# Optimization experiments

Hardware: AMD Instinct MI355X
Metric: run time of the kernel (lower is better)

The kernel has to match this reference:

```python
import jax, jax.numpy as jnp
import numpy as np

B, T, D = 2, 2048, 1024
H = 16
HD = D // H  # head dim == config.k == config.v == 64


def setup_inputs() -> dict:
    key = jax.random.key(0)
    k1, k2, k3 = jax.random.split(key, 3)
    scale = 0.02
    x = jax.random.normal(k1, (B, T, D), dtype=jnp.float32)
    W1 = jax.random.normal(k2, (D, 3 * D), dtype=jnp.float32) * scale
    b1 = jnp.zeros((3 * D,), dtype=jnp.float32)
    W2 = jax.random.normal(k3, (D, D), dtype=jnp.float32) * scale
    b2 = jnp.zeros((D,), dtype=jnp.float32)
    return {"x": x, "W1": W1, "b1": b1, "W2": W2, "b2": b2}


def reference(x, W1, b1, W2, b2):
    # Fused QKV projection (dropout layers are identity in eval mode).
    Bx, Tx, C = x.shape
    qkv = x @ W1 + b1                      # [B, T, 3D]
    q, k, v = jnp.split(qkv, 3, axis=-1)   # each [B, T, D]
    q = q.reshape(Bx, Tx, H, HD).transpose(0, 2, 1, 3)  # [B, H, T, hd]
    k = k.reshape(Bx, Tx, H, HD).transpose(0, 2, 1, 3)
    v = v.reshape(Bx, Tx, H, HD).transpose(0, 2, 1, 3)

    logits = jnp.einsum('bhmk,bhnk->bhmn', q, k) / jnp.sqrt(jnp.float32(HD))
    # causal mask (lower-triangular bias buffer)
    causal = jnp.tril(jnp.ones((Tx, Tx), dtype=bool))
    logits = jnp.where(causal[None, None], logits, jnp.float32(-jnp.inf))
    att = jax.nn.softmax(logits, axis=-1)   # [B, H, T, T]

    y = jnp.einsum('bhmn,bhnv->bhmv', att, v)        # [B, H, T, hd]
    y = y.transpose(0, 2, 1, 3).reshape(Bx, Tx, C)   # [B, T, D]
    return y @ W2 + b2
```

## Files before the change

kernel.cpp:

```cpp
#include <hip/hip_runtime.h>

typedef __attribute__((ext_vector_type(8))) short bf16x8;
typedef __attribute__((ext_vector_type(4))) float f32x4;
typedef __attribute__((ext_vector_type(16))) float f32x16;
typedef __attribute__((ext_vector_type(4))) short short4v;
typedef __attribute__((ext_vector_type(4))) unsigned int uint4v;

#define B_  2
#define T_  2048
#define D_  1024
#define H_  16
#define HD_ 64

__device__ inline short f2bf(float f){
  unsigned u = __builtin_bit_cast(unsigned, f);
  u += 0x7fff + ((u >> 16) & 1);
  return (short)(u >> 16);
}
__device__ inline float bf2f(short s){
  unsigned u = ((unsigned)(unsigned short)s) << 16;
  return __builtin_bit_cast(float, u);
}

__device__ inline void gl2lds16(const void* g, void* l){
  __builtin_amdgcn_global_load_lds(
      (const __attribute__((address_space(1))) unsigned int*)g,
      (__attribute__((address_space(3))) unsigned int*)l, 16, 0, 0);
}

__device__ inline void transpose_tile(const float* __restrict__ in,
                                      short* __restrict__ out,
                                      int R, int C, int bx, int by){
  __shared__ float tile[32][33];
  int tx = threadIdx.x & 31, ty0 = threadIdx.x >> 5;
#pragma unroll
  for (int i = 0; i < 4; i++){
    int ty = ty0 + i * 8;
    tile[ty][tx] = in[(by + ty) * C + bx + tx];
  }
  __syncthreads();
#pragma unroll
  for (int i = 0; i < 4; i++){
    int ty = ty0 + i * 8;
    out[(bx + ty) * R + by + tx] = f2bf(tile[tx][ty]);
  }
}

__global__ __launch_bounds__(256) void prep(
    const float* __restrict__ x,  short* __restrict__ xb,
    const float* __restrict__ W1, short* __restrict__ W1T,
    const float* __restrict__ W2, short* __restrict__ W2T){
  const int bid = blockIdx.x;
  if (bid < 4096){
    int i = (bid * 256 + threadIdx.x) * 4;
    float4 v = *(const float4*)(x + i);
    short4v o;
    o[0] = f2bf(v.x); o[1] = f2bf(v.y); o[2] = f2bf(v.z); o[3] = f2bf(v.w);
    *(short4v*)(xb + i) = o;
  } else if (bid < 4096 + 3072){
    int tb = bid - 4096;
    transpose_tile(W1, W1T, 1024, 3072, (tb % 96) << 5, (tb / 96) << 5);
  } else {
    int tb = bid - 7168;
    transpose_tile(W2, W2T, 1024, 1024, (tb % 32) << 5, (tb / 32) << 5);
  }
}

#define QSCALE 0.18033688011112042f

__global__ __launch_bounds__(512) void gemm_qkv8(
    const short* __restrict__ A, const short* __restrict__ Bt,
    const float* __restrict__ bias,
    short* __restrict__ q, short* __restrict__ kk, short* __restrict__ vT){
  constexpr int K_ = 1024, NT = K_ / 64;
  __shared__ short As[2][256 * 64];
  __shared__ short Bs[2][256 * 64];
  const int tid = threadIdx.x;
  const int lane = tid & 63, w = tid >> 6;
  const int wm = w >> 2, wn = w & 3;
  const int lr = lane & 15, lk = lane >> 4;
  const int brow = blockIdx.y * 256, bcol = blockIdx.x * 256;
  const short* Ag = A  + brow * K_;
  const short* Bg = Bt + bcol * K_;
  f32x4 acc[8][4] = {};

  auto stageA = [&](int buf, int k0){
#pragma unroll
    for (int j = 0; j < 4; j++){
      int row = wm * 128 + wn * 32 + j * 8 + (lane >> 3);
      int colb = (lane & 7) * 16;
      int cs = colb ^ ((row & 7) << 4);
      gl2lds16(Ag + row * K_ + k0 + (cs >> 1), (char*)As[buf] + row * 128 + colb);
    }
  };
  auto stageB = [&](int buf, int k0){
#pragma unroll
    for (int j = 0; j < 4; j++){
      int row = (wn >> 1) * 128 + (wm * 2 + (wn & 1)) * 32 + j * 8 + (lane >> 3);
      int colb = (lane & 7) * 16;
      int cs = colb ^ ((row & 7) << 4);
      gl2lds16(Bg + row * K_ + k0 + (cs >> 1), (char*)Bs[buf] + row * 128 + colb);
    }
  };

  bf16x8 aF[8], bF[4], bF2[4];
  auto loadA = [&](const short* Ac, int r){
#pragma unroll
    for (int mf = 0; mf < 4; mf++){
      int row = wm * 128 + r * 64 + mf * 16 + lr;
      const char* rp = (const char*)Ac + row * 128;
      int swz = (row & 7) << 4;
#pragma unroll
      for (int kx = 0; kx < 2; kx++)
        aF[mf * 2 + kx] = *(const bf16x8*)(rp + ((kx * 64 + lk * 16) ^ swz));
    }
  };
  auto loadB = [&](const short* Bc, int c, bf16x8* dst){
#pragma unroll
    for (int nf = 0; nf < 2; nf++){
      int row = wn * 64 + c * 32 + nf * 16 + lr;
      const char* rp = (const char*)Bc + row * 128;
      int swz = (row & 7) << 4;
#pragma unroll
      for (int kx = 0; kx < 2; kx++)
        dst[nf * 2 + kx] = *(const bf16x8*)(rp + ((kx * 64 + lk * 16) ^ swz));
    }
  };

#define MFMA_SUB(r, c, B)                                                    \
  __builtin_amdgcn_s_setprio(1);                                             \
  _Pragma("unroll")                                                          \
  for (int mf = 0; mf < 4; mf++)                                             \
    _Pragma("unroll")                                                        \
    for (int nf = 0; nf < 2; nf++)                                           \
      _Pragma("unroll")                                                      \
      for (int kx = 0; kx < 2; kx++)                                         \
        acc[(r)*4 + mf][(c)*2 + nf] = __builtin_amdgcn_mfma_f32_16x16x32_bf16(\
            aF[mf*2+kx], (B)[nf*2+kx], acc[(r)*4 + mf][(c)*2 + nf], 0, 0, 0);\
  __builtin_amdgcn_s_setprio(0);

  stageA(0, 0);
  stageB(0, 0);

  for (int t = 0; t < NT; ++t){
    const int cur = t & 1, nxt = cur ^ 1;
    const short* Ac = As[cur];
    const short* Bc = Bs[cur];
    const bool pf = (t + 1 < NT);
    asm volatile("s_waitcnt vmcnt(0)" ::: "memory");
    __builtin_amdgcn_s_barrier();
    __builtin_amdgcn_sched_barrier(0);
    loadA(Ac, 0);
    loadB(Bc, 0, bF);
    if (pf) stageA(nxt, (t + 1) * 64);
    __builtin_amdgcn_sched_barrier(0);
    __builtin_amdgcn_s_barrier();
    __builtin_amdgcn_sched_barrier(0);
    MFMA_SUB(0, 0, bF)
    __builtin_amdgcn_sched_barrier(0);
    __builtin_amdgcn_s_barrier();
    loadB(Bc, 1, bF2);
    if (pf) stageB(nxt, (t + 1) * 64);
    __builtin_amdgcn_sched_barrier(0);
    __builtin_amdgcn_s_barrier();
    __builtin_amdgcn_sched_barrier(0);
    MFMA_SUB(0, 1, bF2)
    __builtin_amdgcn_sched_barrier(0);
    __builtin_amdgcn_s_barrier();
    loadA(Ac, 1);
    __builtin_amdgcn_sched_barrier(0);
    __builtin_amdgcn_s_barrier();
    __builtin_amdgcn_sched_barrier(0);
    MFMA_SUB(1, 0, bF)
    __builtin_amdgcn_sched_barrier(0);
    __builtin_amdgcn_s_barrier();
    MFMA_SUB(1, 1, bF2)
    __builtin_amdgcn_sched_barrier(0);
  }

#pragma unroll
  for (int nf = 0; nf < 4; nf++){
    int n = bcol + wn * 64 + nf * 16 + lr;
    float bv = bias[n];
    int sec = n >> 10, d = n & 1023, h = d >> 6, hd = d & 63;
#pragma unroll
    for (int qd = 0; qd < 8; qd++){
      int m0 = brow + wm * 128 + qd * 16 + lk * 4;
      int bb = m0 >> 11, t0 = m0 & 2047;
      int bh = bb * H_ + h;
      if (sec == 0){
#pragma unroll
        for (int r = 0; r < 4; r++)
          q[(bh * T_ + t0 + r) * HD_ + hd] = f2bf((acc[qd][nf][r] + bv) * QSCALE);
      } else if (sec == 1){
#pragma unroll
        for (int r = 0; r < 4; r++)
          kk[(bh * T_ + t0 + r) * HD_ + hd] = f2bf(acc[qd][nf][r] + bv);
      } else {
        float v0 = acc[qd][nf][0] + bv, v1 = acc[qd][nf][1] + bv;
        float v2 = acc[qd][nf][2] + bv, v3 = acc[qd][nf][3] + bv;
        unsigned lo = (unsigned)(unsigned short)f2bf(v0) | ((unsigned)(unsigned short)f2bf(v1) << 16);
        unsigned hi = (unsigned)(unsigned short)f2bf(v2) | ((unsigned)(unsigned short)f2bf(v3) << 16);
        uint2 pk; pk.x = lo; pk.y = hi;
        *(uint2*)(vT + (bh * HD_ + hd) * T_ + t0) = pk;
      }
    }
  }
}

#define BM 128
#define BN 128
#define BK 32

template<int N_, int K_>
__global__ __launch_bounds__(256, 3) void gemm_bt(
    const short* __restrict__ A, const short* __restrict__ Bt,
    const float* __restrict__ bias, float* __restrict__ outf){
  __shared__ short As[3][BM * BK];
  __shared__ short Bs[3][BN * BK];
  const int tid = threadIdx.x;
  const int lane = tid & 63, w = tid >> 6;
  const int wm = w >> 1, wn = w & 1;
  const int lr = lane & 15, lk = lane >> 4;
  const int brow = blockIdx.y * BM, bcol = blockIdx.x * BN;
  f32x4 acc[4][4] = {};
  const short* Ag = A  + brow * K_;
  const short* Bg = Bt + bcol * K_;

  auto stage = [&](int buf, int k0){
#pragma unroll
    for (int i = 0; i < 2; i++){
      int idx = i * 256 + tid;
      int row = idx >> 2, c8 = (idx & 3) * 8;
      gl2lds16(Ag + row * K_ + k0 + c8, (char*)As[buf] + idx * 16);
      gl2lds16(Bg + row * K_ + k0 + c8, (char*)Bs[buf] + idx * 16);
    }
  };

  const int NT = K_ / BK;
  stage(0, 0);
  stage(1, BK);
  for (int t = 0; t < NT; ++t){
    if (t + 1 < NT)
      asm volatile("s_waitcnt vmcnt(4)" ::: "memory");
    else
      asm volatile("s_waitcnt vmcnt(0)" ::: "memory");
    __builtin_amdgcn_s_barrier();
    __builtin_amdgcn_sched_barrier(0);
    if (t + 2 < NT)
      stage((t + 2) % 3, (t + 2) * BK);
    __builtin_amdgcn_sched_barrier(0);

    const short* Ac = As[t % 3];
    const short* Bc = Bs[t % 3];
    bf16x8 a[4], b[4];
#pragma unroll
    for (int mf = 0; mf < 4; mf++)
      a[mf] = *(const bf16x8*)(Ac + (wm * 64 + mf * 16 + lr) * BK + lk * 8);
#pragma unroll
    for (int nf = 0; nf < 4; nf++)
      b[nf] = *(const bf16x8*)(Bc + (wn * 64 + nf * 16 + lr) * BK + lk * 8);
    __builtin_amdgcn_s_setprio(1);
#pragma unroll
    for (int mf = 0; mf < 4; mf++)
#pragma unroll
      for (int nf = 0; nf < 4; nf++)
        acc[mf][nf] = __builtin_amdgcn_mfma_f32_16x16x32_bf16(a[mf], b[nf], acc[mf][nf], 0, 0, 0);
    __builtin_amdgcn_s_setprio(0);
  }

#pragma unroll
  for (int nf = 0; nf < 4; nf++){
    int n = bcol + wn * 64 + nf * 16 + lr;
    float bv = bias[n];
#pragma unroll
    for (int mf = 0; mf < 4; mf++){
      int m0 = brow + wm * 64 + mf * 16 + lk * 4;
#pragma unroll
      for (int r = 0; r < 4; r++)
        outf[(m0 + r) * N_ + n] = acc[mf][nf][r] + bv;
    }
  }
}

__device__ inline int crow(int r, int h){ return (r & 3) + 8 * (r >> 2) + 4 * h; }

template<int NS>
__global__ __launch_bounds__(256, 4) void attn32(
    const short* __restrict__ Q, const short* __restrict__ Kg,
    const short* __restrict__ Vt, short* __restrict__ Y,
    short* __restrict__ Op, float* __restrict__ ml){
  __shared__ short Ks[2][64 * 64];
  __shared__ short Vs[2][64 * 64];
  __shared__ float bounce[4][32];
  const int tid = threadIdx.x;
  const int w = tid >> 6, l = tid & 63;
  const int lq = l & 31, h = l >> 5;
  const int bx = blockIdx.x;
  int i, hf;
  if constexpr (NS == 4){
    int u = bx >> 5, v = u & 15;
    i = (v < 8) ? 15 - v : v - 8;
    hf = u >> 4;
  } else {
    i = (bx < 256) ? 15 - (bx >> 5) : (bx >> 5) - 8;
    hf = 0;
  }
  const int bh = bx & 31;
  const int q0 = i * 128, qw = q0 + w * 32;
  const int nt = 2 * (i + 1);
  const int t0 = hf * nt / NS;
  const int t1 = (hf + 1) * nt / NS;

  bf16x8 qb[4];
  {
    const short* qbase = Q + (bh * T_ + qw + lq) * HD_;
#pragma unroll
    for (int dk = 0; dk < 4; dk++)
      qb[dk] = *(const bf16x8*)(qbase + dk * 16 + h * 8);
  }

  f32x16 o0 = {}, o1 = {};
  float m = -1e30f, ll = 0.f;

  auto stage = [&](int buf, int t){
#pragma unroll
    for (int j = 0; j < 2; j++){
      int idx = j * 256 + tid;
      int row = idx >> 3, cb = (idx & 7) * 16;
      int cbs = cb ^ ((row & 7) << 4);
      gl2lds16(Kg + (bh * T_ + t * 64 + row) * HD_ + (cbs >> 1), (char*)Ks[buf] + idx * 16);
      gl2lds16(Vt + (bh * HD_ + row) * T_ + t * 64 + (cbs >> 1), (char*)Vs[buf] + idx * 16);
    }
  };

  if (t0 < t1){
    stage(0, t0);
    for (int t = t0; t < t1; ++t){
      const int cur = (t - t0) & 1;
      if (t + 1 < t1){
        stage(cur ^ 1, t + 1);
        asm volatile("s_waitcnt vmcnt(4)" ::: "memory");
      } else {
        asm volatile("s_waitcnt vmcnt(0)" ::: "memory");
      }
      __builtin_amdgcn_s_barrier();
      __builtin_amdgcn_sched_barrier(0);

      const int kvb = t * 64;
      if (kvb <= qw + 31){
        const short* Kc = Ks[cur];
        const short* Vc = Vs[cur];

        f32x16 s[2] = {};
        __builtin_amdgcn_s_setprio(1);
#pragma unroll
        for (int kb = 0; kb < 2; kb++){
          int row = kb * 32 + lq;
          const char* rp = (const char*)Kc + row * 128;
          int swz = (row & 7) << 4;
#pragma unroll
          for (int dk = 0; dk < 4; dk++){
            bf16x8 ka = *(const bf16x8*)(rp + ((dk * 32 + h * 16) ^ swz));
            s[kb] = __builtin_amdgcn_mfma_f32_32x32x16_bf16(ka, qb[dk], s[kb], 0, 0, 0);
          }
        }
        __builtin_amdgcn_s_setprio(0);

        const int qg = qw + lq;
        if (kvb + 63 > qw){
#pragma unroll
          for (int kb = 0; kb < 2; kb++)
#pragma unroll
            for (int r = 0; r < 16; r++){
              int kv = kvb + kb * 32 + crow(r, h);
              if (kv > qg) s[kb][r] = -1e30f;
            }
        }

        float pm = s[0][0];
#pragma unroll
        for (int r = 1; r < 16; r++) pm = fmaxf(pm, s[0][r]);
#pragma unroll
        for (int r = 0; r < 16; r++) pm = fmaxf(pm, s[1][r]);
        pm = fmaxf(pm, __shfl_xor(pm, 32));

        if (__any(pm > m + 8.f)){
          float mn = fmaxf(pm, m);
          float sf = __builtin_amdgcn_exp2f(m - mn);
          m = mn;
          ll *= sf;
          bounce[w][lq] = sf;
#pragma unroll
          for (int r = 0; r < 16; r++){
            float sr = bounce[w][crow(r, h)];
            o0[r] *= sr; o1[r] *= sr;
          }
        }

        float ts = 0.f;
#pragma unroll
        for (int kb = 0; kb < 2; kb++)
#pragma unroll
          for (int r = 0; r < 16; r++){
            float p = __builtin_amdgcn_exp2f(s[kb][r] - m);
            s[kb][r] = p;
            ts += p;
          }
        ts += __shfl_xor(ts, 32);
        ll += ts;

        unsigned pw0[8], pw1[8];
#pragma unroll
        for (int kb = 0; kb < 2; kb++)
#pragma unroll
          for (int gg = 0; gg < 4; gg++){
            unsigned r0, r1;
            asm("v_cvt_pk_bf16_f32 %0, %1, %2" : "=v"(r0) : "v"(s[kb][gg * 4 + 0]), "v"(s[kb][gg * 4 + 1]));
            asm("v_cvt_pk_bf16_f32 %0, %1, %2" : "=v"(r1) : "v"(s[kb][gg * 4 + 2]), "v"(s[kb][gg * 4 + 3]));
            pw0[kb * 4 + gg] = r0;
            pw1[kb * 4 + gg] = r1;
          }
#pragma unroll
        for (int ks = 0; ks < 4; ks++){
          asm("v_permlane32_swap_b32 %0, %1" : "+v"(pw0[2 * ks]), "+v"(pw0[2 * ks + 1]));
          asm("v_permlane32_swap_b32 %0, %1" : "+v"(pw1[2 * ks]), "+v"(pw1[2 * ks + 1]));
        }

        __builtin_amdgcn_s_setprio(1);
#pragma unroll
        for (int ks = 0; ks < 4; ks++){
          uint4v paw;
          paw[0] = pw0[2 * ks];     paw[1] = pw1[2 * ks];
          paw[2] = pw0[2 * ks + 1]; paw[3] = pw1[2 * ks + 1];
          bf16x8 pa = __builtin_bit_cast(bf16x8, paw);
#pragma unroll
          for (int nb = 0; nb < 2; nb++){
            int row = nb * 32 + lq;
            bf16x8 vb = *(const bf16x8*)((const char*)Vc + row * 128 +
                          ((ks * 32 + h * 16) ^ ((row & 7) << 4)));
            if (nb == 0) o0 = __builtin_amdgcn_mfma_f32_32x32x16_bf16(pa, vb, o0, 0, 0, 0);
            else         o1 = __builtin_amdgcn_mfma_f32_32x32x16_bf16(pa, vb, o1, 0, 0, 0);
          }
        }
        __builtin_amdgcn_s_setprio(0);
      }
      __builtin_amdgcn_sched_barrier(0);
      __builtin_amdgcn_s_barrier();
    }
  }

  if constexpr (NS == 4){
    short* Oq = Op + ((size_t)(hf * 32 + bh)) * (size_t)T_ * 64;
    if (h == 0){
      float* mlr = ml + ((size_t)(hf * 32 + bh) * T_ + (qw + lq)) * 2;
      mlr[0] = m; mlr[1] = ll;
    }
#pragma unroll
    for (int r = 0; r < 16; r++){
      int qg = qw + crow(r, h);
      Oq[qg * 64 + lq]      = f2bf(o0[r]);
      Oq[qg * 64 + 32 + lq] = f2bf(o1[r]);
    }
  } else {
    bounce[w][lq] = __builtin_amdgcn_rcpf(ll);
    const int b = bh >> 4, hh = bh & 15;
#pragma unroll
    for (int r = 0; r < 16; r++){
      int row = crow(r, h);
      float rl = bounce[w][row];
      int qg = qw + row;
      short* yb = Y + (b * T_ + qg) * D_ + hh * 64;
      yb[lq]      = f2bf(o0[r] * rl);
      yb[32 + lq] = f2bf(o1[r] * rl);
    }
  }
}

__global__ __launch_bounds__(256) void attn_merge(
    const short* __restrict__ Op, const float* __restrict__ ml,
    short* __restrict__ Y){
  int gid = blockIdx.x * 256 + threadIdx.x;
  int rid = gid >> 2, c16 = (gid & 3) * 16;
  float mh[4], lh[4];
#pragma unroll
  for (int hf = 0; hf < 4; hf++){
    float2 v = *(const float2*)(ml + (size_t)hf * 131072 + rid * 2);
    mh[hf] = v.x; lh[hf] = v.y;
  }
  float M = fmaxf(fmaxf(mh[0], mh[1]), fmaxf(mh[2], mh[3]));
  float f[4], den = 0.f;
#pragma unroll
  for (int hf = 0; hf < 4; hf++){
    f[hf] = __builtin_amdgcn_exp2f(mh[hf] - M);
    den += f[hf] * lh[hf];
  }
  float rl = 1.f / den;
  float acc[16] = {};
#pragma unroll
  for (int hf = 0; hf < 4; hf++){
    const short* o = Op + (size_t)hf * 4194304 + (size_t)rid * 64 + c16;
    bf16x8 a = *(const bf16x8*)(o);
    bf16x8 b = *(const bf16x8*)(o + 8);
    float fh = f[hf];
#pragma unroll
    for (int j = 0; j < 8; j++){
      acc[j]     += fh * bf2f(a[j]);
      acc[8 + j] += fh * bf2f(b[j]);
    }
  }
  int bh = rid >> 11, t = rid & 2047;
  short* yb = Y + (((bh >> 4) * T_ + t) * D_) + (bh & 15) * 64 + c16;
  bf16x8 o0, o1;
#pragma unroll
  for (int j = 0; j < 8; j++){
    o0[j] = f2bf(acc[j] * rl);
    o1[j] = f2bf(acc[8 + j] * rl);
  }
  *(bf16x8*)(yb)     = o0;
  *(bf16x8*)(yb + 8) = o1;
}

extern "C" void kernel_launch(void* const* d_in, const int* in_sizes, int n_in,
                              void* d_out, int out_size, void* d_ws, size_t ws_size,
                              hipStream_t stream) {
  const float* x  = (const float*)d_in[0];
  const float* W1 = (const float*)d_in[1];
  const float* b1 = (const float*)d_in[2];
  const float* W2 = (const float*)d_in[3];
  const float* b2 = (const float*)d_in[4];
  float* out = (float*)d_out;

  char* ws = (char*)d_ws;
  short* W1T = (short*)(ws);
  short* W2T = (short*)(ws + 6291456);
  short* xb  = (short*)(ws + 8388608);
  short* q   = (short*)(ws + 16777216);
  short* kk  = (short*)(ws + 25165824);
  short* vT  = (short*)(ws + 33554432);
  short* Op  = (short*)(ws + 41943040);
  float* mlb = (float*)(ws);
  short* y   = xb;

  const size_t need = 41943040ull + 33554432ull;
  const bool split = ws_size >= need;

  prep<<<dim3(8192), dim3(256), 0, stream>>>(x, xb, W1, W1T, W2, W2T);
  gemm_qkv8<<<dim3(12, 16), dim3(512), 0, stream>>>(xb, W1T, b1, q, kk, vT);
  if (split){
    attn32<4><<<dim3(2048), dim3(256), 0, stream>>>(q, kk, vT, nullptr, Op, mlb);
    attn_merge<<<dim3(1024), dim3(256), 0, stream>>>(Op, mlb, y);
  } else {
    attn32<1><<<dim3(512), dim3(256), 0, stream>>>(q, kk, vT, y, nullptr, nullptr);
  }
  gemm_bt<1024, 1024><<<dim3(8, 32), dim3(256), 0, stream>>>(y, W2T, b2, out);
}
```

Measured before the change: 114.9 us.

## Restructure QKV GEMM into finer-grained half-tile staging with counted vmcnt waits

The QKV projection GEMM main loop is rewritten as an 8-iteration, two-stage unrolled schedule. Global-to-LDS staging is split into half-tile units issued across the MFMA phases, and a dummy LDS buffer absorbs the out-of-range prefetches at the tail, so the loop needs no branch. The full vmcnt(0) drain each k-step becomes partial vmcnt(4) waits, which keeps loads in flight across iterations. This adds an extra LDS buffer, which may reduce occupancy, and makes the barrier schedule more intricate, with a risk of subtle ordering hazards.

```diff
diff --git a/kernel.cpp b/kernel.cpp
--- a/kernel.cpp
+++ b/kernel.cpp
@@ -72,9 +72,10 @@
     const short* __restrict__ A, const short* __restrict__ Bt,
     const float* __restrict__ bias,
     short* __restrict__ q, short* __restrict__ kk, short* __restrict__ vT){
-  constexpr int K_ = 1024, NT = K_ / 64;
+  constexpr int K_ = 1024, NT = 16, NITER = 8;
   __shared__ short As[2][256 * 64];
   __shared__ short Bs[2][256 * 64];
+  __shared__ short Dm[128 * 64];
   const int tid = threadIdx.x;
   const int lane = tid & 63, w = tid >> 6;
   const int wm = w >> 2, wn = w & 3;
@@ -83,27 +84,34 @@
   const short* Ag = A  + brow * K_;
   const short* Bg = Bt + bcol * K_;
   f32x4 acc[8][4] = {};
-
-  auto stageA = [&](int buf, int k0){
-#pragma unroll
-    for (int j = 0; j < 4; j++){
-      int row = wm * 128 + wn * 32 + j * 8 + (lane >> 3);
-      int colb = (lane & 7) * 16;
+  bf16x8 aF[8], bFc0[4], bFc1[4];
+
+  auto unitA = [&](int s, int h, int kt){
+    const bool dm = kt >= NT;
+    const int k0 = (dm ? NT - 1 : kt) * 64;
+#pragma unroll
+    for (int j = 0; j < 2; j++){
+      int idx = j * 512 + tid;
+      int row = h * 128 + (idx >> 3);
+      int colb = (idx & 7) * 16;
       int cs = colb ^ ((row & 7) << 4);
-      gl2lds16(Ag + row * K_ + k0 + (cs >> 1), (char*)As[buf] + row * 128 + colb);
+      char* dst = dm ? ((char*)Dm + idx * 16) : ((char*)As[s] + row * 128 + colb);
+      gl2lds16(Ag + row * K_ + k0 + (cs >> 1), dst);
     }
   };
-  auto stageB = [&](int buf, int k0){
-#pragma unroll
-    for (int j = 0; j < 4; j++){
-      int row = (wn >> 1) * 128 + (wm * 2 + (wn & 1)) * 32 + j * 8 + (lane >> 3);
-      int colb = (lane & 7) * 16;
+  auto unitB = [&](int s, int h, int kt){
+    const bool dm = kt >= NT;
+    const int k0 = (dm ? NT - 1 : kt) * 64;
+#pragma unroll
+    for (int j = 0; j < 2; j++){
+      int idx = j * 512 + tid;
+      int row = h * 128 + (idx >> 3);
+      int colb = (idx & 7) * 16;
       int cs = colb ^ ((row & 7) << 4);
-      gl2lds16(Bg + row * K_ + k0 + (cs >> 1), (char*)Bs[buf] + row * 128 + colb);
+      char* dst = dm ? ((char*)Dm + idx * 16) : ((char*)Bs[s] + row * 128 + colb);
+      gl2lds16(Bg + row * K_ + k0 + (cs >> 1), dst);
     }
   };
-
-  bf16x8 aF[8], bF[4], bF2[4];
   auto loadA = [&](const short* Ac, int r){
 #pragma unroll
     for (int mf = 0; mf < 4; mf++){
@@ -127,8 +135,7 @@
     }
   };
 
-#define MFMA_SUB(r, c, B)                                                    \
-  __builtin_amdgcn_s_setprio(1);                                             \
+#define MFMA16(r, c, B)                                                      \
   _Pragma("unroll")                                                          \
   for (int mf = 0; mf < 4; mf++)                                             \
     _Pragma("unroll")                                                        \
@@ -136,69 +143,78 @@
       _Pragma("unroll")                                                      \
       for (int kx = 0; kx < 2; kx++)                                         \
         acc[(r)*4 + mf][(c)*2 + nf] = __builtin_amdgcn_mfma_f32_16x16x32_bf16(\
-            aF[mf*2+kx], (B)[nf*2+kx], acc[(r)*4 + mf][(c)*2 + nf], 0, 0, 0);\
-  __builtin_amdgcn_s_setprio(0);
-
-  stageA(0, 0);
-  stageB(0, 0);
-
-  for (int t = 0; t < NT; ++t){
-    const int cur = t & 1, nxt = cur ^ 1;
-    const short* Ac = As[cur];
-    const short* Bc = Bs[cur];
-    const bool pf = (t + 1 < NT);
-    asm volatile("s_waitcnt vmcnt(0)" ::: "memory");
-    __builtin_amdgcn_s_barrier();
-    __builtin_amdgcn_sched_barrier(0);
-    loadA(Ac, 0);
-    loadB(Bc, 0, bF);
-    if (pf) stageA(nxt, (t + 1) * 64);
-    __builtin_amdgcn_sched_barrier(0);
-    __builtin_amdgcn_s_barrier();
-    __builtin_amdgcn_sched_barrier(0);
-    MFMA_SUB(0, 0, bF)
-    __builtin_amdgcn_sched_barrier(0);
-    __builtin_amdgcn_s_barrier();
-    loadB(Bc, 1, bF2);
-    if (pf) stageB(nxt, (t + 1) * 64);
-    __builtin_amdgcn_sched_barrier(0);
-    __builtin_amdgcn_s_barrier();
-    __builtin_amdgcn_sched_barrier(0);
-    MFMA_SUB(0, 1, bF2)
-    __builtin_amdgcn_sched_barrier(0);
-    __builtin_amdgcn_s_barrier();
-    loadA(Ac, 1);
-    __builtin_amdgcn_sched_barrier(0);
-    __builtin_amdgcn_s_barrier();
-    __builtin_amdgcn_sched_barrier(0);
-    MFMA_SUB(1, 0, bF)
-    __builtin_amdgcn_sched_barrier(0);
-    __builtin_amdgcn_s_barrier();
-    MFMA_SUB(1, 1, bF2)
-    __builtin_amdgcn_sched_barrier(0);
-  }
-
-#pragma unroll
-  for (int nf = 0; nf < 4; nf++){
-    int n = bcol + wn * 64 + nf * 16 + lr;
+            aF[mf*2+kx], (B)[nf*2+kx], acc[(r)*4 + mf][(c)*2 + nf], 0, 0, 0);
+
+#define PHASE_TAIL(R, C, BREG, GATE)                                         \
+  __builtin_amdgcn_sched_barrier(0);                                         \
+  __builtin_amdgcn_s_barrier();                                              \
+  asm volatile("s_waitcnt lgkmcnt(0)" ::: "memory");                         \
+  __builtin_amdgcn_sched_barrier(0);                                         \
+  __builtin_amdgcn_s_setprio(1);                                             \
+  MFMA16(R, C, BREG)                                                         \
+  __builtin_amdgcn_s_setprio(0);                                             \
+  __builtin_amdgcn_sched_barrier(0);                                         \
+  if (GATE) asm volatile("s_waitcnt vmcnt(4)" ::: "memory");                 \
+  __builtin_amdgcn_s_barrier();                                              \
+  __builtin_amdgcn_sched_barrier(0);
+
+  unitB(0, 0, 0); unitB(0, 1, 0);
+  unitA(0, 0, 0); unitA(0, 1, 0);
+  unitB(1, 0, 1); unitB(1, 1, 1);
+  asm volatile("s_waitcnt vmcnt(4)" ::: "memory");
+  __builtin_amdgcn_s_barrier();
+  __builtin_amdgcn_sched_barrier(0);
+
+  for (int it = 0; it < NITER; ++it){
+    const int kA1 = 2 * it + 1;
+    const int kS0 = 2 * it + 2;
+    const int kB1 = 2 * it + 3;
+    loadA(As[0], 0); loadB(Bs[0], 0, bFc0);
+    unitA(1, 0, kA1);
+    PHASE_TAIL(0, 0, bFc0, false)
+    loadB(Bs[0], 1, bFc1);
+    unitA(1, 1, kA1);
+    PHASE_TAIL(0, 1, bFc1, false)
+    loadA(As[0], 1);
+    unitB(0, 0, kS0);
+    PHASE_TAIL(1, 0, bFc0, false)
+    unitB(0, 1, kS0);
+    PHASE_TAIL(1, 1, bFc1, true)
+    loadA(As[1], 0); loadB(Bs[1], 0, bFc0);
+    unitA(0, 0, kS0);
+    PHASE_TAIL(0, 0, bFc0, false)
+    loadB(Bs[1], 1, bFc1);
+    unitA(0, 1, kS0);
+    PHASE_TAIL(0, 1, bFc1, false)
+    loadA(As[1], 1);
+    unitB(1, 0, kB1);
+    PHASE_TAIL(1, 0, bFc0, false)
+    unitB(1, 1, kB1);
+    PHASE_TAIL(1, 1, bFc1, true)
+  }
+  asm volatile("s_waitcnt vmcnt(0)" ::: "memory");
+
+#pragma unroll
+  for (int cn = 0; cn < 4; cn++){
+    int n = bcol + wn * 64 + (cn >> 1) * 32 + (cn & 1) * 16 + lr;
     float bv = bias[n];
-    int sec = n >> 10, d = n & 1023, h = d >> 6, hd = d & 63;
-#pragma unroll
-    for (int qd = 0; qd < 8; qd++){
-      int m0 = brow + wm * 128 + qd * 16 + lk * 4;
+    int sec = n >> 10, d = n & 1023, hh = d >> 6, hd = d & 63;
+#pragma unroll
+    for (int a = 0; a < 8; a++){
+      int m0 = brow + wm * 128 + (a >> 2) * 64 + (a & 3) * 16 + lk * 4;
       int bb = m0 >> 11, t0 = m0 & 2047;
-      int bh = bb * H_ + h;
+      int bh = bb * H_ + hh;
       if (sec == 0){
 #pragma unroll
         for (int r = 0; r < 4; r++)
-          q[(bh * T_ + t0 + r) * HD_ + hd] = f2bf((acc[qd][nf][r] + bv) * QSCALE);
+          q[(bh * T_ + t0 + r) * HD_ + hd] = f2bf((acc[a][cn][r] + bv) * QSCALE);
       } else if (sec == 1){
 #pragma unroll
         for (int r = 0; r < 4; r++)
-          kk[(bh * T_ + t0 + r) * HD_ + hd] = f2bf(acc[qd][nf][r] + bv);
+          kk[(bh * T_ + t0 + r) * HD_ + hd] = f2bf(acc[a][cn][r] + bv);
       } else {
-        float v0 = acc[qd][nf][0] + bv, v1 = acc[qd][nf][1] + bv;
-        float v2 = acc[qd][nf][2] + bv, v3 = acc[qd][nf][3] + bv;
+        float v0 = acc[a][cn][0] + bv, v1 = acc[a][cn][1] + bv;
+        float v2 = acc[a][cn][2] + bv, v3 = acc[a][cn][3] + bv;
         unsigned lo = (unsigned)(unsigned short)f2bf(v0) | ((unsigned)(unsigned short)f2bf(v1) << 16);
         unsigned hi = (unsigned)(unsigned short)f2bf(v2) | ((unsigned)(unsigned short)f2bf(v3) << 16);
         uint2 pk; pk.x = lo; pk.y = hi;
```

Result: no change. 114.0 us (-0.8%).
